# Kernel optimization log

Hardware: AMD Instinct MI355X
Metric: run time of the kernel (lower is better)

## Reference

```python
import jax, jax.numpy as jnp
import numpy as np

E = 2      # expansion
G = 8      # groups
K = 128    # num_clusters
N = 1024   # feature_size (dim)
D = E * N // G  # per-group cluster dim = 256
EPS = 1e-12


def _l2norm(v, axis):
    return v / jnp.maximum(jnp.linalg.norm(v, axis=axis, keepdims=True), EPS)


def setup_inputs() -> dict:
    key = jax.random.key(0)
    ks = jax.random.split(key, 8)
    x = jax.random.normal(ks[0], (64, N, 8, 8), dtype=jnp.float32)
    W_inp = jax.random.normal(ks[1], (E * N, N), dtype=jnp.float32) * 0.02
    b_inp = jax.random.uniform(ks[2], (E * N,), dtype=jnp.float32)
    W_g = jax.random.normal(ks[3], (G, E * N), dtype=jnp.float32) * 0.02
    b_g = jax.random.uniform(ks[4], (G,), dtype=jnp.float32)
    W_gk = jax.random.normal(ks[5], (G * K, E * N), dtype=jnp.float32) * 0.02
    b_gk = jax.random.uniform(ks[6], (G * K,), dtype=jnp.float32)
    centroids = jax.random.normal(ks[7], (K, D), dtype=jnp.float32) * 0.1
    return {"x": x, "W_inp": W_inp, "b_inp": b_inp, "W_g": W_g, "b_g": b_g,
            "W_gk": W_gk, "b_gk": b_gk, "centroids": centroids}


def reference(x, W_inp, b_inp, W_g, b_g, W_gk, b_gk, centroids):
    b8, c, h, w = x.shape
    bs = b8 // 8
    # [bs*8, C, H, W] -> [bs, M=8*H*W, N=C]
    x = x.reshape(bs, 8, c, h, w).transpose(0, 2, 1, 3, 4).reshape(bs, c, 8 * h * w)
    x = jnp.transpose(x, (0, 2, 1))            # [bs, M, N]
    M = x.shape[1]
    x = _l2norm(x, axis=2)                     # normalize_input
    x = x @ W_inp.T + b_inp                    # [bs, M, E*N]
    alpha_g = jax.nn.sigmoid(x @ W_g.T + b_g)  # [bs, M, G]
    # NOTE: original uses Softmax(dim=1) -> softmax over token dim M
    alpha_gk = jax.nn.softmax(x @ W_gk.T + b_gk, axis=1)   # [bs, M, G*K]
    alpha_gk = alpha_gk.reshape(bs, M, G, K)
    xr = x.reshape(bs, M, G, D)
    w_full = alpha_g[..., None] * alpha_gk     # [bs, M, G, K]
    # vlad[b,k,d] = sum_{m,g} w*(x - c) = einsum(w,x) - (sum w) * c
    vlad = jnp.einsum('bmgk,bmgd->bkd', w_full, xr) \
        - jnp.sum(w_full, axis=(1, 2))[..., None] * centroids  # [bs, K, D]
    vlad = _l2norm(vlad, axis=-1).reshape(bs, K * D)
    return _l2norm(vlad, axis=1)
```

## Files before the change

### kernel.cpp

```cpp
#include <hip/hip_runtime.h>
#include <hip/hip_bf16.h>
#include <math.h>

#define EPSN 1e-12f
typedef unsigned short ushort_t;

typedef float f32x4 __attribute__((ext_vector_type(4)));
typedef short s16x8 __attribute__((ext_vector_type(8)));
typedef unsigned short u16x8 __attribute__((ext_vector_type(8)));
typedef unsigned short u16x4 __attribute__((ext_vector_type(4)));

__device__ __forceinline__ void gload_lds16(const void* g, void* l) {
  __builtin_amdgcn_global_load_lds((const __attribute__((address_space(1))) void*)g,
                                   (__attribute__((address_space(3))) void*)l, 16, 0, 0);
}

__global__ void k0_ssq(const float* __restrict__ x, float* __restrict__ ssq8) {
  int b8 = blockIdx.x >> 3;
  int cc = blockIdx.x & 7;
  int t = threadIdx.x;
  int s4 = (t & 15) * 4;
  int cg = t >> 4;
  const float* xp = x + (size_t)b8 * 65536 + (size_t)cc * 128 * 64;
  float4 a = {0.f, 0.f, 0.f, 0.f};
#pragma unroll
  for (int j = 0; j < 8; ++j) {
    int c = cg + j * 16;
    float4 v = *(const float4*)(xp + (size_t)c * 64 + s4);
    a.x = fmaf(v.x, v.x, a.x);
    a.y = fmaf(v.y, v.y, a.y);
    a.z = fmaf(v.z, v.z, a.z);
    a.w = fmaf(v.w, v.w, a.w);
  }
  __shared__ float red[16][68];
  *(float4*)&red[cg][s4] = a;
  __syncthreads();
  if (t < 64) {
    float s = 0.f;
#pragma unroll
    for (int g = 0; g < 16; ++g) s += red[g][t];
    ssq8[cc * 4096 + b8 * 64 + t] = s;
  }
}

__global__ void k1_transpose(const float* __restrict__ x, const float* __restrict__ ssq8,
                             __hip_bfloat16* __restrict__ xnb) {
  int ct = blockIdx.x;
  int b8 = blockIdx.y;
  int t = threadIdx.x;
  __shared__ float tile[64][65];
  __shared__ float ivs[64];
  if (t < 64) {
    float s = 0.f;
#pragma unroll
    for (int cc = 0; cc < 8; ++cc) s += ssq8[cc * 4096 + b8 * 64 + t];
    ivs[t] = rsqrtf(fmaxf(s, 1e-24f));
  }
  int s = t & 63, cq = t >> 6;
  const float* xp = x + (size_t)b8 * 65536 + (size_t)ct * 64 * 64;
#pragma unroll
  for (int r = 0; r < 16; ++r) {
    int cl = cq * 16 + r;
    tile[cl][s] = xp[cl * 64 + s];
  }
  __syncthreads();
  int cl = t & 63, sq = t >> 6;
#pragma unroll
  for (int r = 0; r < 16; ++r) {
    int smm = sq * 16 + r;
    int tm = b8 * 64 + smm;
    xnb[(size_t)tm * 1024 + ct * 64 + cl] = __float2bfloat16(tile[cl][smm] * ivs[smm]);
  }
}

__global__ void kpack2(const float* __restrict__ Wi, const float* __restrict__ Wgk,
                       const float* __restrict__ W_g, const float* __restrict__ b_inp,
                       const float* __restrict__ b_g, __hip_bfloat16* __restrict__ oWi,
                       __hip_bfloat16* __restrict__ oWx, float* __restrict__ bWg) {
  int bid = blockIdx.x;
  int t = threadIdx.x;
  if (bid < 2048) {
    int i = (bid * 256 + t) * 4;
    float4 v = *(const float4*)(Wi + i);
    oWi[i + 0] = __float2bfloat16(v.x);
    oWi[i + 1] = __float2bfloat16(v.y);
    oWi[i + 2] = __float2bfloat16(v.z);
    oWi[i + 3] = __float2bfloat16(v.w);
  } else if (bid < 4096) {
    int i = ((bid - 2048) * 256 + t) * 4;
    float4 v = *(const float4*)(Wgk + i);
    oWx[i + 0] = __float2bfloat16(v.x);
    oWx[i + 1] = __float2bfloat16(v.y);
    oWx[i + 2] = __float2bfloat16(v.z);
    oWx[i + 3] = __float2bfloat16(v.w);
  } else if (bid < 4112) {
    int i = (bid - 4096) * 1024 + t * 4;
    float4 v = *(const float4*)(W_g + i);
    __hip_bfloat16* o = oWx + 1024 * 2048 + i;
    o[0] = __float2bfloat16(v.x);
    o[1] = __float2bfloat16(v.y);
    o[2] = __float2bfloat16(v.z);
    o[3] = __float2bfloat16(v.w);
  } else if (bid < 4352) {
    int i = (bid - 4112) * 1024 + t * 4;
    ushort_t* o = (ushort_t*)(oWx + 1032 * 2048) + i;
    *(u16x4*)o = (u16x4){0, 0, 0, 0};
  } else {
    int j = bid - 4352;
    const float* row = W_g + (size_t)j * 2048;
    float s = 0.f;
    for (int c = t; c < 2048; c += 256) s = fmaf(b_inp[c], row[c], s);
    __shared__ float red[256];
    red[t] = s;
    __syncthreads();
    for (int o = 128; o > 0; o >>= 1) {
      if (t < o) red[t] += red[t + o];
      __syncthreads();
    }
    if (t == 0) bWg[j] = red[0] + b_g[j];
  }
}

template <int OUT>
__launch_bounds__(512, 4)
__global__ void gemm_bf16_nt_db(const ushort_t* __restrict__ A, const ushort_t* __restrict__ B,
                                ushort_t* __restrict__ Cb, float* __restrict__ Cf,
                                ushort_t* __restrict__ Tt, int K, int N) {
  __shared__ alignas(16) ushort_t SH[32768];
  const int tid = threadIdx.x;
  const int m0 = blockIdx.y * 128, n0 = blockIdx.x * 128;
  const int w = tid >> 6, l = tid & 63;
  const int wr = w >> 2, wc = w & 3;
  const int srow = w * 8 + (l >> 3);
  const int ksw = ((l & 7) ^ (l >> 3)) * 8;
  const ushort_t* Ag0 = A + (size_t)(m0 + srow) * K + ksw;
  const ushort_t* Ag1 = A + (size_t)(m0 + 64 + srow) * K + ksw;
  const ushort_t* Bg0 = B + (size_t)(n0 + srow) * K + ksw;
  const ushort_t* Bg1 = B + (size_t)(n0 + 64 + srow) * K + ksw;
  const int l0 = w * 512;
  const int l1 = 4096 + w * 512;

  f32x4 acc[4][2];
#pragma unroll
  for (int i = 0; i < 4; ++i)
#pragma unroll
    for (int j = 0; j < 2; ++j) acc[i][j] = (f32x4){0.f, 0.f, 0.f, 0.f};

  const int sw = l & 7, qq = l >> 4;

#define ASH(buf) (SH + (buf)*8192)
#define BSH(buf) (SH + 16384 + (buf)*8192)
#define STAGE(buf, k0)                               \
  {                                                  \
    gload_lds16(Ag0 + (k0), ASH(buf) + l0);          \
    gload_lds16(Ag1 + (k0), ASH(buf) + l1);          \
    gload_lds16(Bg0 + (k0), BSH(buf) + l0);          \
    gload_lds16(Bg1 + (k0), BSH(buf) + l1);          \
  }

#define COMPUTE(buf)                                                                     \
  {                                                                                      \
    s16x8 af[4][2], bf[2][2];                                                            \
    _Pragma("unroll") for (int kk = 0; kk < 2; ++kk) {                                   \
      int slot = (((kk << 2) + qq) ^ sw) * 8;                                            \
      _Pragma("unroll") for (int mi = 0; mi < 4; ++mi)                                   \
          af[mi][kk] = *(const s16x8*)&ASH(buf)[(wr * 64 + mi * 16 + (l & 15)) * 64 +    \
                                               slot];                                   \
      _Pragma("unroll") for (int ni = 0; ni < 2; ++ni)                                   \
          bf[ni][kk] = *(const s16x8*)&BSH(buf)[(wc * 32 + ni * 16 + (l & 15)) * 64 +    \
                                               slot];                                   \
    }                                                                                    \
    _Pragma("unroll") for (int kk = 0; kk < 2; ++kk)                                     \
        _Pragma("unroll") for (int mi = 0; mi < 4; ++mi)                                 \
            _Pragma("unroll") for (int ni = 0; ni < 2; ++ni)                             \
                acc[mi][ni] = __builtin_amdgcn_mfma_f32_16x16x32_bf16(af[mi][kk],        \
                                                                     bf[ni][kk],        \
                                                                     acc[mi][ni], 0, 0, 0); \
  }

  const int nt = K >> 6;
  STAGE(0, 0);
  int buf = 0;
  for (int t = 0; t < nt - 1; ++t) {
    STAGE(buf ^ 1, (t + 1) << 6);
    asm volatile("s_waitcnt vmcnt(4)" ::: "memory");
    __builtin_amdgcn_s_barrier();
    asm volatile("" ::: "memory");
    COMPUTE(buf);
    asm volatile("" ::: "memory");
    __builtin_amdgcn_s_barrier();
    buf ^= 1;
  }
  asm volatile("s_waitcnt vmcnt(0)" ::: "memory");
  __builtin_amdgcn_s_barrier();
  asm volatile("" ::: "memory");
  COMPUTE(buf);
#undef STAGE
#undef COMPUTE
#undef ASH
#undef BSH

  if constexpr (OUT == 1) {
#pragma unroll
    for (int mi = 0; mi < 4; ++mi) {
      int row = m0 + wr * 64 + mi * 16 + (l >> 4) * 4;
#pragma unroll
      for (int ni = 0; ni < 2; ++ni) {
        int col = n0 + wc * 32 + ni * 16 + (l & 15);
#pragma unroll
        for (int r = 0; r < 4; ++r)
          Cf[(size_t)(row + r) * N + col] = acc[mi][ni][r];
      }
    }
  } else if constexpr (OUT == 2) {
#pragma unroll
    for (int mi = 0; mi < 4; ++mi) {
      int row = m0 + wr * 64 + mi * 16 + (l >> 4) * 4;
#pragma unroll
      for (int ni = 0; ni < 2; ++ni) {
        int col = n0 + wc * 32 + ni * 16 + (l & 15);
#pragma unroll
        for (int r = 0; r < 4; ++r) {
          __hip_bfloat16 hb = __float2bfloat16(acc[mi][ni][r]);
          Cb[(size_t)(row + r) * N + col] = *(ushort_t*)&hb;
        }
      }
    }
  } else {
    __syncthreads();
    ushort_t* T = SH + w * 2304;
#pragma unroll
    for (int mi = 0; mi < 4; ++mi) {
      int m = mi * 16 + (l >> 4) * 4;
#pragma unroll
      for (int ni = 0; ni < 2; ++ni) {
        int c = ni * 16 + (l & 15);
        u16x4 pk;
#pragma unroll
        for (int r = 0; r < 4; ++r) {
          __hip_bfloat16 hb = __float2bfloat16(acc[mi][ni][r]);
          pk[r] = *(ushort_t*)&hb;
        }
        *(u16x4*)&T[c * 72 + m] = pk;
        int row = m0 + wr * 64 + m;
        int col = n0 + wc * 32 + c;
#pragma unroll
        for (int r = 0; r < 4; ++r) Cb[(size_t)(row + r) * N + col] = pk[r];
      }
    }
    int cb = l >> 3, mc = (l & 7) ^ cb;
#pragma unroll
    for (int j = 0; j < 4; ++j) {
      int c = cb + j * 8;
      u16x8 v = *(const u16x8*)&T[c * 72 + mc * 8];
      *(u16x8*)&Tt[(size_t)(n0 + wc * 32 + c) * 4096 + m0 + wr * 64 + mc * 8] = v;
    }
  }
}

__launch_bounds__(256)
__global__ void k5_softmax(const ushort_t* __restrict__ logitsTb, const float* __restrict__ bWg,
                           float* __restrict__ colsumW, ushort_t* __restrict__ wbT) {
  int wv = (blockIdx.x << 2) + (threadIdx.x >> 6);
  int q = wv >> 3, b = wv & 7;
  int l = threadIdx.x & 63;
  int g = q >> 7;
  size_t base = (size_t)q * 4096 + b * 512 + l * 8;
  u16x8 v8 = *(const u16x8*)(logitsTb + base);
  float vs[8];
#pragma unroll
  for (int i = 0; i < 8; ++i) vs[i] = __uint_as_float(((unsigned)v8[i]) << 16);
  float M = vs[0];
#pragma unroll
  for (int i = 1; i < 8; ++i) M = fmaxf(M, vs[i]);
#pragma unroll
  for (int m = 1; m < 64; m <<= 1) M = fmaxf(M, __shfl_xor(M, m, 64));
  float e[8], S = 0.f;
#pragma unroll
  for (int i = 0; i < 8; ++i) {
    e[i] = expf(vs[i] - M);
    S += e[i];
  }
#pragma unroll
  for (int m = 1; m < 64; m <<= 1) S += __shfl_xor(S, m, 64);
  float R = 1.0f / S;
  u16x8 g8 = *(const u16x8*)(logitsTb + (size_t)(1024 + g) * 4096 + b * 512 + l * 8);
  float bg = bWg[g];
  float wv8[8], wsum = 0.f;
#pragma unroll
  for (int i = 0; i < 8; ++i) {
    float gl = __uint_as_float(((unsigned)g8[i]) << 16);
    float ag = 1.0f / (1.0f + expf(-(gl + bg)));
    wv8[i] = e[i] * R * ag;
    wsum += wv8[i];
  }
#pragma unroll
  for (int m = 1; m < 64; m <<= 1) wsum += __shfl_xor(wsum, m, 64);
  if (l == 0) colsumW[b * 1024 + q] = wsum;
  u16x8 o;
#pragma unroll
  for (int i = 0; i < 8; ++i) {
    __hip_bfloat16 hb = __float2bfloat16(wv8[i]);
    o[i] = *(ushort_t*)&hb;
  }
  *(u16x8*)(wbT + base) = o;
}

__launch_bounds__(256)
__global__ void k6_vlad_mfma(const ushort_t* __restrict__ wbT, const ushort_t* __restrict__ YcT,
                             float* __restrict__ vpart) {
  int kt = blockIdx.x >> 2, dt = blockIdx.x & 3;
  int ms = blockIdx.y, b = blockIdx.z;
  __shared__ alignas(16) ushort_t Ash[2][4096];
  __shared__ alignas(16) ushort_t Bsh[2][4096];
  const int tid = threadIdx.x;
  const int w = tid >> 6, l = tid & 63;
  const int wr = w >> 1, wc = w & 1;
  const int crow = l >> 3;
  const int ksw = ((l & 7) ^ crow) * 8;

  const ushort_t* Ap[2];
  const ushort_t* Bp[2];
  int loff[2];
#pragma unroll
  for (int c = 0; c < 2; ++c) {
    int chunk = w * 2 + c;
    Ap[c] = wbT + (size_t)(kt * 64 + chunk * 8 + crow) * 4096 + b * 512 + ms * 64 + ksw;
    Bp[c] = YcT + (size_t)(dt * 64 + chunk * 8 + crow) * 4096 + b * 512 + ms * 64 + ksw;
    loff[c] = chunk * 512;
  }

  f32x4 acc[2][2];
#pragma unroll
  for (int i = 0; i < 2; ++i)
#pragma unroll
    for (int j = 0; j < 2; ++j) acc[i][j] = (f32x4){0.f, 0.f, 0.f, 0.f};

  const int sw = l & 7, qq = l >> 4;

#define STAGE6(buf, g)                                                       \
  {                                                                          \
    size_t offA = (size_t)(g)*524288;                                        \
    size_t offB = (size_t)(g)*1048576;                                       \
    gload_lds16(Ap[0] + offA, &Ash[buf][loff[0]]);                           \
    gload_lds16(Ap[1] + offA, &Ash[buf][loff[1]]);                           \
    gload_lds16(Bp[0] + offB, &Bsh[buf][loff[0]]);                           \
    gload_lds16(Bp[1] + offB, &Bsh[buf][loff[1]]);                           \
  }

#define COMPUTE6(buf)                                                                    \
  {                                                                                      \
    s16x8 af[2][2], bf[2][2];                                                            \
    _Pragma("unroll") for (int kk = 0; kk < 2; ++kk) {                                   \
      int slot = (((kk << 2) + qq) ^ sw) * 8;                                            \
      _Pragma("unroll") for (int mi = 0; mi < 2; ++mi) {                                 \
        af[mi][kk] = *(const s16x8*)&Ash[buf][(wr * 32 + mi * 16 + (l & 15)) * 64 +      \
                                             slot];                                     \
        bf[mi][kk] = *(const s16x8*)&Bsh[buf][(wc * 32 + mi * 16 + (l & 15)) * 64 +      \
                                             slot];                                     \
      }                                                                                  \
    }                                                                                    \
    _Pragma("unroll") for (int kk = 0; kk < 2; ++kk)                                     \
        _Pragma("unroll") for (int mi = 0; mi < 2; ++mi)                                 \
            _Pragma("unroll") for (int ni = 0; ni < 2; ++ni)                             \
                acc[mi][ni] = __builtin_amdgcn_mfma_f32_16x16x32_bf16(af[mi][kk],        \
                                                                     bf[ni][kk],        \
                                                                     acc[mi][ni], 0, 0, 0); \
  }

  STAGE6(0, 0);
  int buf = 0;
  for (int s = 0; s < 7; ++s) {
    STAGE6(buf ^ 1, s + 1);
    asm volatile("s_waitcnt vmcnt(4)" ::: "memory");
    __builtin_amdgcn_s_barrier();
    asm volatile("" ::: "memory");
    COMPUTE6(buf);
    asm volatile("" ::: "memory");
    __builtin_amdgcn_s_barrier();
    buf ^= 1;
  }
  asm volatile("s_waitcnt vmcnt(0)" ::: "memory");
  __builtin_amdgcn_s_barrier();
  asm volatile("" ::: "memory");
  COMPUTE6(buf);
#undef STAGE6
#undef COMPUTE6

#pragma unroll
  for (int mi = 0; mi < 2; ++mi) {
    int row = kt * 64 + wr * 32 + mi * 16 + (l >> 4) * 4;
#pragma unroll
    for (int ni = 0; ni < 2; ++ni) {
      int col = dt * 64 + wc * 32 + ni * 16 + (l & 15);
#pragma unroll
      for (int r = 0; r < 4; ++r)
        vpart[((size_t)(ms * 8 + b) * 128 + row + r) * 256 + col] = acc[mi][ni][r];
    }
  }
}

__global__ void k7_intranorm(const float* __restrict__ vpart, const float* __restrict__ colsumW,
                             const float* __restrict__ b_inp, const float* __restrict__ cent,
                             float* __restrict__ out, float* __restrict__ ss1) {
  int k = blockIdx.x;
  int b = blockIdx.y;
  int d = threadIdx.x;
  float S = 0.f, bp = 0.f;
#pragma unroll
  for (int g = 0; g < 8; ++g) {
    float cw = colsumW[b * 1024 + g * 128 + k];
    S += cw;
    bp = fmaf(b_inp[g * 256 + d], cw, bp);
  }
  size_t off = ((size_t)b * 128 + k) * 256 + d;
  float v = bp - S * cent[(size_t)k * 256 + d];
#pragma unroll
  for (int i = 0; i < 8; ++i) v += vpart[off + (size_t)i * 262144];
  float ss = v * v;
#pragma unroll
  for (int m = 1; m < 64; m <<= 1) ss += __shfl_xor(ss, m, 64);
  __shared__ float red[4];
  int lane = d & 63, wv = d >> 6;
  if (lane == 0) red[wv] = ss;
  __syncthreads();
  float tot = red[0] + red[1] + red[2] + red[3];
  float rinv = 1.0f / fmaxf(sqrtf(tot), EPSN);
  out[off] = v * rinv;
  if (d == 0) ss1[b * 128 + k] = tot * rinv * rinv;
}

__global__ void k8_finalnorm(const float* __restrict__ ss1, float* __restrict__ out) {
  int b = blockIdx.x;
  int t = threadIdx.x;
  __shared__ float red[256];
  red[t] = (t < 128) ? ss1[b * 128 + t] : 0.f;
  __syncthreads();
  for (int o = 128; o > 0; o >>= 1) {
    if (t < o) red[t] += red[t + o];
    __syncthreads();
  }
  float rinv = 1.0f / fmaxf(sqrtf(red[0]), EPSN);
  float* op = out + (size_t)b * 32768;
  for (int i = t; i < 32768; i += 256) op[i] *= rinv;
}

extern "C" void kernel_launch(void* const* d_in, const int* in_sizes, int n_in,
                              void* d_out, int out_size, void* d_ws, size_t ws_size,
                              hipStream_t stream) {
  const float* x     = (const float*)d_in[0];
  const float* W_inp = (const float*)d_in[1];
  const float* b_inp = (const float*)d_in[2];
  const float* W_g   = (const float*)d_in[3];
  const float* b_g   = (const float*)d_in[4];
  const float* W_gk  = (const float*)d_in[5];
  const float* cent  = (const float*)d_in[7];
  float* out = (float*)d_out;
  float* ws = (float*)d_ws;

  float* ssq8    = ws + 0;
  float* colsumW = ws + 32768;
  float* ss1     = ws + 40960;
  float* bWg     = ws + 41984;
  __hip_bfloat16* xnb = (__hip_bfloat16*)(ws + 42048);
  ushort_t* wbT  = (ushort_t*)xnb;
  __hip_bfloat16* Wib  = (__hip_bfloat16*)(ws + 2139200);
  __hip_bfloat16* Wgkx = (__hip_bfloat16*)(ws + 3187776);
  float* vpart   = ws + 2139200;
  __hip_bfloat16* Ycb  = (__hip_bfloat16*)(ws + 4367424);
  ushort_t* YcT  = (ushort_t*)(ws + 6464576);
  ushort_t* logitsTb = (ushort_t*)(ws + 10658880);

  k0_ssq<<<512, 256, 0, stream>>>(x, ssq8);
  k1_transpose<<<dim3(16, 64), 256, 0, stream>>>(x, ssq8, xnb);
  kpack2<<<4360, 256, 0, stream>>>(W_inp, W_gk, W_g, b_inp, b_g, Wib, Wgkx, bWg);
  gemm_bf16_nt_db<0><<<dim3(16, 32), 512, 0, stream>>>((const ushort_t*)xnb, (const ushort_t*)Wib,
                                                       (ushort_t*)Ycb, nullptr, YcT, 1024, 2048);
  gemm_bf16_nt_db<2><<<dim3(32, 9), 512, 0, stream>>>((const ushort_t*)Wgkx, (const ushort_t*)Ycb,
                                                      logitsTb, nullptr, nullptr, 2048, 4096);
  k5_softmax<<<2048, 256, 0, stream>>>(logitsTb, bWg, colsumW, wbT);
  k6_vlad_mfma<<<dim3(8, 8, 8), 256, 0, stream>>>(wbT, YcT, vpart);
  k7_intranorm<<<dim3(128, 8), 256, 0, stream>>>(vpart, colsumW, b_inp, cent, out, ss1);
  k8_finalnorm<<<8, 256, 0, stream>>>(ss1, out);
}
```

Baseline: 122.1 us.

## Precompose gating/cluster weights with input projection to shrink logits GEMM K

Instead of computing logits as (W_gk|W_g)·Y where Y = xn·W_inp^T (K=2048), the weights are precomposed into Wcomb = (W_gk|W_g)·W_inp (a small 1152x1024 GEMM), so the logits GEMM runs directly on the normalized input with K=1024. The Y projection is now computed directly in transposed form (W_inp·xn^T) so the fused transpose-store epilogue is dropped. The weight-product GEMM is weight-only work that is repeated each call, and the extra bf16 rounding of Wcomb changes numerics slightly.

```diff
diff --git a/kernel.cpp b/kernel.cpp
--- a/kernel.cpp
+++ b/kernel.cpp
@@ -76,7 +76,8 @@
 __global__ void kpack2(const float* __restrict__ Wi, const float* __restrict__ Wgk,
                        const float* __restrict__ W_g, const float* __restrict__ b_inp,
                        const float* __restrict__ b_g, __hip_bfloat16* __restrict__ oWi,
-                       __hip_bfloat16* __restrict__ oWx, float* __restrict__ bWg) {
+                       __hip_bfloat16* __restrict__ oWx, ushort_t* __restrict__ oWibT,
+                       float* __restrict__ bWg) {
   int bid = blockIdx.x;
   int t = threadIdx.x;
   if (bid < 2048) {
@@ -105,7 +106,7 @@
     int i = (bid - 4112) * 1024 + t * 4;
     ushort_t* o = (ushort_t*)(oWx + 1032 * 2048) + i;
     *(u16x4*)o = (u16x4){0, 0, 0, 0};
-  } else {
+  } else if (bid < 4360) {
     int j = bid - 4352;
     const float* row = W_g + (size_t)j * 2048;
     float s = 0.f;
@@ -118,14 +119,39 @@
       __syncthreads();
     }
     if (t == 0) bWg[j] = red[0] + b_g[j];
-  }
-}
-
-template <int OUT>
+  } else {
+    int tt = bid - 4360;
+    int cp0 = (tt >> 4) * 64;
+    int c0 = (tt & 15) * 64;
+    __shared__ ushort_t tile[64][72];
+    int r = t >> 2, cs = (t & 3) * 16;
+    const float* src = Wi + (size_t)(cp0 + r) * 1024 + c0 + cs;
+#pragma unroll
+    for (int j = 0; j < 16; j += 4) {
+      float4 v = *(const float4*)(src + j);
+      __hip_bfloat16 h0 = __float2bfloat16(v.x), h1 = __float2bfloat16(v.y);
+      __hip_bfloat16 h2 = __float2bfloat16(v.z), h3 = __float2bfloat16(v.w);
+      tile[r][cs + j + 0] = *(ushort_t*)&h0;
+      tile[r][cs + j + 1] = *(ushort_t*)&h1;
+      tile[r][cs + j + 2] = *(ushort_t*)&h2;
+      tile[r][cs + j + 3] = *(ushort_t*)&h3;
+    }
+    __syncthreads();
+    int c = t >> 2, ms = (t & 3) * 16;
+    u16x8 o0, o1;
+#pragma unroll
+    for (int j = 0; j < 8; ++j) o0[j] = tile[ms + j][c];
+#pragma unroll
+    for (int j = 0; j < 8; ++j) o1[j] = tile[ms + 8 + j][c];
+    ushort_t* dst = oWibT + (size_t)(c0 + c) * 2048 + cp0 + ms;
+    *(u16x8*)dst = o0;
+    *(u16x8*)(dst + 8) = o1;
+  }
+}
+
 __launch_bounds__(512, 4)
-__global__ void gemm_bf16_nt_db(const ushort_t* __restrict__ A, const ushort_t* __restrict__ B,
-                                ushort_t* __restrict__ Cb, float* __restrict__ Cf,
-                                ushort_t* __restrict__ Tt, int K, int N) {
+__global__ void gemm_nt_bf16(const ushort_t* __restrict__ A, const ushort_t* __restrict__ B,
+                             ushort_t* __restrict__ C, int K, int N) {
   __shared__ alignas(16) ushort_t SH[32768];
   const int tid = threadIdx.x;
   const int m0 = blockIdx.y * 128, n0 = blockIdx.x * 128;
@@ -200,60 +226,17 @@
 #undef ASH
 #undef BSH
 
-  if constexpr (OUT == 1) {
-#pragma unroll
-    for (int mi = 0; mi < 4; ++mi) {
-      int row = m0 + wr * 64 + mi * 16 + (l >> 4) * 4;
-#pragma unroll
-      for (int ni = 0; ni < 2; ++ni) {
-        int col = n0 + wc * 32 + ni * 16 + (l & 15);
-#pragma unroll
-        for (int r = 0; r < 4; ++r)
-          Cf[(size_t)(row + r) * N + col] = acc[mi][ni][r];
+#pragma unroll
+  for (int mi = 0; mi < 4; ++mi) {
+    int row = m0 + wr * 64 + mi * 16 + (l >> 4) * 4;
+#pragma unroll
+    for (int ni = 0; ni < 2; ++ni) {
+      int col = n0 + wc * 32 + ni * 16 + (l & 15);
+#pragma unroll
+      for (int r = 0; r < 4; ++r) {
+        __hip_bfloat16 hb = __float2bfloat16(acc[mi][ni][r]);
+        C[(size_t)(row + r) * N + col] = *(ushort_t*)&hb;
       }
-    }
-  } else if constexpr (OUT == 2) {
-#pragma unroll
-    for (int mi = 0; mi < 4; ++mi) {
-      int row = m0 + wr * 64 + mi * 16 + (l >> 4) * 4;
-#pragma unroll
-      for (int ni = 0; ni < 2; ++ni) {
-        int col = n0 + wc * 32 + ni * 16 + (l & 15);
-#pragma unroll
-        for (int r = 0; r < 4; ++r) {
-          __hip_bfloat16 hb = __float2bfloat16(acc[mi][ni][r]);
-          Cb[(size_t)(row + r) * N + col] = *(ushort_t*)&hb;
-        }
-      }
-    }
-  } else {
-    __syncthreads();
-    ushort_t* T = SH + w * 2304;
-#pragma unroll
-    for (int mi = 0; mi < 4; ++mi) {
-      int m = mi * 16 + (l >> 4) * 4;
-#pragma unroll
-      for (int ni = 0; ni < 2; ++ni) {
-        int c = ni * 16 + (l & 15);
-        u16x4 pk;
-#pragma unroll
-        for (int r = 0; r < 4; ++r) {
-          __hip_bfloat16 hb = __float2bfloat16(acc[mi][ni][r]);
-          pk[r] = *(ushort_t*)&hb;
-        }
-        *(u16x4*)&T[c * 72 + m] = pk;
-        int row = m0 + wr * 64 + m;
-        int col = n0 + wc * 32 + c;
-#pragma unroll
-        for (int r = 0; r < 4; ++r) Cb[(size_t)(row + r) * N + col] = pk[r];
-      }
-    }
-    int cb = l >> 3, mc = (l & 7) ^ cb;
-#pragma unroll
-    for (int j = 0; j < 4; ++j) {
-      int c = cb + j * 8;
-      u16x8 v = *(const u16x8*)&T[c * 72 + mc * 8];
-      *(u16x8*)&Tt[(size_t)(n0 + wc * 32 + c) * 4096 + m0 + wr * 64 + mc * 8] = v;
     }
   }
 }
@@ -465,19 +448,22 @@
   __hip_bfloat16* xnb = (__hip_bfloat16*)(ws + 42048);
   ushort_t* wbT  = (ushort_t*)xnb;
   __hip_bfloat16* Wib  = (__hip_bfloat16*)(ws + 2139200);
-  __hip_bfloat16* Wgkx = (__hip_bfloat16*)(ws + 3187776);
+  ushort_t* WibT = (ushort_t*)(ws + 3187776);
   float* vpart   = ws + 2139200;
-  __hip_bfloat16* Ycb  = (__hip_bfloat16*)(ws + 4367424);
-  ushort_t* YcT  = (ushort_t*)(ws + 6464576);
-  ushort_t* logitsTb = (ushort_t*)(ws + 10658880);
+  __hip_bfloat16* Wgkx   = (__hip_bfloat16*)(ws + 4236352);
+  __hip_bfloat16* Wcombx = (__hip_bfloat16*)(ws + 5416000);
+  ushort_t* YcT  = (ushort_t*)(ws + 6005824);
+  ushort_t* logitsTb = (ushort_t*)(ws + 10200128);
 
   k0_ssq<<<512, 256, 0, stream>>>(x, ssq8);
   k1_transpose<<<dim3(16, 64), 256, 0, stream>>>(x, ssq8, xnb);
-  kpack2<<<4360, 256, 0, stream>>>(W_inp, W_gk, W_g, b_inp, b_g, Wib, Wgkx, bWg);
-  gemm_bf16_nt_db<0><<<dim3(16, 32), 512, 0, stream>>>((const ushort_t*)xnb, (const ushort_t*)Wib,
-                                                       (ushort_t*)Ycb, nullptr, YcT, 1024, 2048);
-  gemm_bf16_nt_db<2><<<dim3(32, 9), 512, 0, stream>>>((const ushort_t*)Wgkx, (const ushort_t*)Ycb,
-                                                      logitsTb, nullptr, nullptr, 2048, 4096);
+  kpack2<<<4872, 256, 0, stream>>>(W_inp, W_gk, W_g, b_inp, b_g, Wib, Wgkx, WibT, bWg);
+  gemm_nt_bf16<<<dim3(8, 9), 512, 0, stream>>>((const ushort_t*)Wgkx, WibT,
+                                               (ushort_t*)Wcombx, 2048, 1024);
+  gemm_nt_bf16<<<dim3(32, 16), 512, 0, stream>>>((const ushort_t*)Wib, (const ushort_t*)xnb,
+                                                 YcT, 1024, 4096);
+  gemm_nt_bf16<<<dim3(32, 9), 512, 0, stream>>>((const ushort_t*)Wcombx, (const ushort_t*)xnb,
+                                                logitsTb, 1024, 4096);
   k5_softmax<<<2048, 256, 0, stream>>>(logitsTb, bWg, colsumW, wbT);
   k6_vlad_mfma<<<dim3(8, 8, 8), 256, 0, stream>>>(wbT, YcT, vpart);
   k7_intranorm<<<dim3(128, 8), 256, 0, stream>>>(vpart, colsumW, b_inp, cent, out, ss1);
```

Measured after the change: 128.1 us. 4.9% more time.
